# Performance work log

Hardware: AMD Instinct MI355X
Metric: run time of the kernel (lower is better)

Reference implementation:

```python
import jax, jax.numpy as jnp
import numpy as np

N_NODES = 100000
IN_DIM = 128
OUT_DIM = 128


def setup_inputs() -> dict:
    key = jax.random.key(0)
    ks = jax.random.split(key, 10)
    # entry counts must be multiples of the edge arity (shape)
    e1, e2, e3 = 300000, 600000, 600000  # arities 1, 2, 3 -> 300k/300k/200k hyperedges
    return {
        "x": jax.random.normal(ks[0], (N_NODES, IN_DIM), dtype=jnp.float32),
        "edge_idx_r1": jax.random.randint(ks[1], (2, e1), 0, N_NODES, dtype=jnp.int32),
        "edge_idx_r2": jax.random.randint(ks[2], (2, e2), 0, N_NODES, dtype=jnp.int32),
        "edge_idx_r3": jax.random.randint(ks[3], (2, e3), 0, N_NODES, dtype=jnp.int32),
        "A_r1": jax.random.normal(ks[4], (IN_DIM * 1, OUT_DIM), dtype=jnp.float32) * np.sqrt(2.0 / (IN_DIM * 1 + OUT_DIM)),
        "A_r2": jax.random.normal(ks[5], (IN_DIM * 2, OUT_DIM), dtype=jnp.float32) * np.sqrt(2.0 / (IN_DIM * 2 + OUT_DIM)),
        "A_r3": jax.random.normal(ks[6], (IN_DIM * 3, OUT_DIM), dtype=jnp.float32) * np.sqrt(2.0 / (IN_DIM * 3 + OUT_DIM)),
        "C_w": jax.random.normal(ks[7], (OUT_DIM, IN_DIM), dtype=jnp.float32) * (1.0 / np.sqrt(IN_DIM)),
        "C_b": jax.random.normal(ks[8], (OUT_DIM,), dtype=jnp.float32) * 0.01,
    }


def _edge_type_messages(x, edge_idx, A, arity, n_nodes):
    # edge_idx: [2, groups*arity]; row0 = src node ids, row1 reshaped -> dest = col 0
    dest = edge_idx[1].reshape(-1, arity)[:, 0]              # [groups]
    src = x[edge_idx[0]].reshape(-1, x.shape[1] * arity)     # [groups, in_dim*arity]
    msg = src @ A                                            # [groups, out_dim]
    # degree normalization within this edge type (== 1/counts from torch.unique)
    counts = jnp.zeros((n_nodes,), dtype=msg.dtype).at[dest].add(1.0)
    msg = msg * (1.0 / counts[dest])[:, None]
    return dest, msg


def reference(x, edge_idx_r1, edge_idx_r2, edge_idx_r3, A_r1, A_r2, A_r3, C_w, C_b):
    n = x.shape[0]
    agg = jnp.zeros((n, C_w.shape[0]), dtype=x.dtype)
    for ei, A, arity in ((edge_idx_r1, A_r1, 1), (edge_idx_r2, A_r2, 2), (edge_idx_r3, A_r3, 3)):
        dest, msg = _edge_type_messages(x, ei, A, arity, n)
        agg = agg.at[dest].add(msg)
    return x @ C_w.T + C_b + agg
```

## Files before the change

kernel.cpp:

```cpp
#include <hip/hip_runtime.h>

#define N_NODES 100000
#define DIM 128

typedef __attribute__((ext_vector_type(8))) short bf16x8;
typedef __attribute__((ext_vector_type(4))) float f32x4;
typedef __attribute__((ext_vector_type(8))) unsigned short ushort8;

__device__ __forceinline__ unsigned short f2bf(float f) {
    union { float f; unsigned u; } v; v.f = f;
    unsigned u = v.u + 0x7FFFu + ((v.u >> 16) & 1u);
    return (unsigned short)(u >> 16);
}
__device__ __forceinline__ float bl(unsigned u) { return __uint_as_float(u << 16); }
__device__ __forceinline__ float bh(unsigned u) { return __uint_as_float(u & 0xFFFF0000u); }

__device__ __forceinline__ void gload_lds16(const void* g, void* l) {
    __builtin_amdgcn_global_load_lds((const __attribute__((address_space(1))) void*)g,
                                     (__attribute__((address_space(3))) void*)l, 16, 0, 0);
}

__device__ __forceinline__ void acc2(float4& a, uint2 v) {
    a.x += bl(v.x); a.y += bh(v.x); a.z += bl(v.y); a.w += bh(v.y);
}
__device__ __forceinline__ void red4(float4& a) {
    a.x += __shfl_xor(a.x, 32); a.y += __shfl_xor(a.y, 32);
    a.z += __shfl_xor(a.z, 32); a.w += __shfl_xor(a.w, 32);
}
__device__ __forceinline__ uint2 pack4(float4 a) {
    uint2 r;
    r.x = (unsigned)f2bf(a.x) | ((unsigned)f2bf(a.y) << 16);
    r.y = (unsigned)f2bf(a.z) | ((unsigned)f2bf(a.w) << 16);
    return r;
}

__global__ void cvt_count_kernel(const float* __restrict__ x, unsigned short* __restrict__ xb,
                                 int n8, const int* __restrict__ e1d,
                                 const int* __restrict__ e2d, const int* __restrict__ e3d,
                                 int ng1, int ng12, int ngall, int* __restrict__ counts) {
    int i = blockIdx.x * 256 + threadIdx.x;
    if (i < n8) {
        const float4* p = reinterpret_cast<const float4*>(x) + (size_t)i * 2;
        float4 a = p[0], b = p[1];
        ushort8 o;
        o[0] = f2bf(a.x); o[1] = f2bf(a.y); o[2] = f2bf(a.z); o[3] = f2bf(a.w);
        o[4] = f2bf(b.x); o[5] = f2bf(b.y); o[6] = f2bf(b.z); o[7] = f2bf(b.w);
        *reinterpret_cast<ushort8*>(xb + (size_t)i * 8) = o;
    }
    if (i < ng1) atomicAdd(&counts[e1d[i]], 1);
    else if (i < ng12) atomicAdd(&counts[N_NODES + e2d[(size_t)(i - ng1) * 2]], 1);
    else if (i < ngall) atomicAdd(&counts[2 * N_NODES + e3d[(size_t)(i - ng12) * 3]], 1);
}

__global__ void cvt_B_all(const float* __restrict__ A1, const float* __restrict__ A2,
                          const float* __restrict__ A3, const float* __restrict__ Cw,
                          unsigned short* __restrict__ bts) {
    int kg = blockIdx.x;
    int c = threadIdx.x;
    float v;
    int slice, kp;
    if (kg < 128)      { slice = 0; kp = kg; v = A1[(size_t)kg * 128 + c]; }
    else if (kg < 384) { int k = kg - 128; slice = 1 + (k >> 7); kp = k & 127; v = A2[(size_t)k * 128 + c]; }
    else if (kg < 768) { int k = kg - 384; slice = 3 + (k >> 7); kp = k & 127; v = A3[(size_t)k * 128 + c]; }
    else               { int k = kg - 768; slice = 6; kp = k; v = Cw[(size_t)c * 128 + k]; }
    bts[(size_t)slice * 16384 + c * 128 + kp] = f2bf(v);
}

__global__ __launch_bounds__(256) void scan_p1(const int* __restrict__ counts,
                                               int* __restrict__ partials) {
    __shared__ int red[256];
    int type = blockIdx.y, blk = blockIdx.x, tid = threadIdx.x;
    int base = blk * 4096 + tid * 16;
    int s = 0;
#pragma unroll
    for (int j = 0; j < 16; ++j) {
        int i = base + j;
        s += (i < N_NODES) ? counts[(size_t)type * N_NODES + i] : 0;
    }
    red[tid] = s;
    __syncthreads();
    for (int off = 128; off > 0; off >>= 1) {
        if (tid < off) red[tid] += red[tid + off];
        __syncthreads();
    }
    if (tid == 0) partials[type * 32 + blk] = red[0];
}

__global__ __launch_bounds__(256) void scan_p3(const int* __restrict__ counts,
                                               const int* __restrict__ partials,
                                               int* __restrict__ cursor) {
    __shared__ int tsum[256];
    __shared__ int baseoff;
    int type = blockIdx.y, blk = blockIdx.x, tid = threadIdx.x;
    if (tid == 0) {
        int r = 0;
        for (int b = 0; b < blk; ++b) r += partials[type * 32 + b];
        baseoff = r;
    }
    int base = blk * 4096 + tid * 16;
    int v[16];
    int s = 0;
#pragma unroll
    for (int j = 0; j < 16; ++j) {
        int i = base + j;
        v[j] = (i < N_NODES) ? counts[(size_t)type * N_NODES + i] : 0;
        s += v[j];
    }
    tsum[tid] = s;
    __syncthreads();
    for (int off = 1; off < 256; off <<= 1) {
        int t2 = (tid >= off) ? tsum[tid - off] : 0;
        __syncthreads();
        tsum[tid] += t2;
        __syncthreads();
    }
    int run = tsum[tid] - s + baseoff;
#pragma unroll
    for (int j = 0; j < 16; ++j) {
        int i = base + j;
        if (i < N_NODES) cursor[(size_t)type * N_NODES + i] = run;
        run += v[j];
    }
}

__global__ void scatter_all_kernel(const int* __restrict__ e1, const int* __restrict__ e2,
                                   const int* __restrict__ e3, int ne1, int ne2, int ne3,
                                   int ng1, int ng12, int ngall, int* __restrict__ cursor,
                                   int* __restrict__ s1, int2* __restrict__ s2,
                                   int4* __restrict__ s3) {
    int g = blockIdx.x * 256 + threadIdx.x;
    if (g < ng1) {
        int d = e1[ne1 + g];
        s1[atomicAdd(&cursor[d], 1)] = e1[g];
    } else if (g < ng12) {
        int k = g - ng1;
        int d = e2[ne2 + 2 * (size_t)k];
        int2 v; v.x = e2[2 * (size_t)k]; v.y = e2[2 * (size_t)k + 1];
        s2[atomicAdd(&cursor[N_NODES + d], 1)] = v;
    } else if (g < ngall) {
        int k = g - ng12;
        int d = e3[ne3 + 3 * (size_t)k];
        int4 v; v.x = e3[3 * (size_t)k]; v.y = e3[3 * (size_t)k + 1];
        v.z = e3[3 * (size_t)k + 2]; v.w = 0;
        s3[atomicAdd(&cursor[2 * N_NODES + d], 1)] = v;
    }
}

__global__ __launch_bounds__(256) void aggregate_x_kernel(
    const unsigned short* __restrict__ xb,
    const int* __restrict__ s1, const int2* __restrict__ s2, const int4* __restrict__ s3,
    const int* __restrict__ counts, const int* __restrict__ ends,
    unsigned short* __restrict__ gbf)
{
    int d = blockIdx.x * 4 + (threadIdx.x >> 6);
    if (d >= N_NODES) return;
    const int l = threadIdx.x & 63, hw = l >> 5, sl = l & 31;
    float4 a0 = {0,0,0,0}, a1 = {0,0,0,0}, a2 = {0,0,0,0};
    float4 a3 = {0,0,0,0}, a4 = {0,0,0,0}, a5 = {0,0,0,0};

    int c1 = counts[d], c2 = counts[N_NODES + d], c3 = counts[2 * N_NODES + d];
    int e1e = ends[d], e2e = ends[N_NODES + d], e3e = ends[2 * N_NODES + d];

    if (c1) {
        for (int i = e1e - c1 + hw; i < e1e; i += 2) {
            uint2 v = *reinterpret_cast<const uint2*>(xb + (size_t)s1[i] * 128 + sl * 4);
            acc2(a0, v);
        }
        float inv = 1.f / (float)c1;
        a0.x *= inv; a0.y *= inv; a0.z *= inv; a0.w *= inv;
    }
    if (c2) {
        for (int i = e2e - c2 + hw; i < e2e; i += 2) {
            int2 p = s2[i];
            uint2 va = *reinterpret_cast<const uint2*>(xb + (size_t)p.x * 128 + sl * 4);
            uint2 vb = *reinterpret_cast<const uint2*>(xb + (size_t)p.y * 128 + sl * 4);
            acc2(a1, va); acc2(a2, vb);
        }
        float inv = 1.f / (float)c2;
        a1.x *= inv; a1.y *= inv; a1.z *= inv; a1.w *= inv;
        a2.x *= inv; a2.y *= inv; a2.z *= inv; a2.w *= inv;
    }
    if (c3) {
        for (int i = e3e - c3 + hw; i < e3e; i += 2) {
            int4 p = s3[i];
            uint2 va = *reinterpret_cast<const uint2*>(xb + (size_t)p.x * 128 + sl * 4);
            uint2 vb = *reinterpret_cast<const uint2*>(xb + (size_t)p.y * 128 + sl * 4);
            uint2 vc = *reinterpret_cast<const uint2*>(xb + (size_t)p.z * 128 + sl * 4);
            acc2(a3, va); acc2(a4, vb); acc2(a5, vc);
        }
        float inv = 1.f / (float)c3;
        a3.x *= inv; a3.y *= inv; a3.z *= inv; a3.w *= inv;
        a4.x *= inv; a4.y *= inv; a4.z *= inv; a4.w *= inv;
        a5.x *= inv; a5.y *= inv; a5.z *= inv; a5.w *= inv;
    }
    red4(a0); red4(a1); red4(a2); red4(a3); red4(a4); red4(a5);
    if (hw == 0) {
        *reinterpret_cast<uint2*>(gbf + ((size_t)0 * N_NODES + d) * 128 + sl * 4) = pack4(a0);
        *reinterpret_cast<uint2*>(gbf + ((size_t)1 * N_NODES + d) * 128 + sl * 4) = pack4(a1);
        *reinterpret_cast<uint2*>(gbf + ((size_t)2 * N_NODES + d) * 128 + sl * 4) = pack4(a2);
        *reinterpret_cast<uint2*>(gbf + ((size_t)3 * N_NODES + d) * 128 + sl * 4) = pack4(a3);
        *reinterpret_cast<uint2*>(gbf + ((size_t)4 * N_NODES + d) * 128 + sl * 4) = pack4(a4);
        *reinterpret_cast<uint2*>(gbf + ((size_t)5 * N_NODES + d) * 128 + sl * 4) = pack4(a5);
    }
}

__global__ __launch_bounds__(256, 2) void gemm_out_kernel(
    const unsigned short* __restrict__ xb, const unsigned short* __restrict__ gbf,
    const unsigned short* __restrict__ bts, const float* __restrict__ Cb,
    float* __restrict__ out, int nnodes)
{
    __shared__ __align__(16) char smem[65536];

    const int tid = threadIdx.x;
    const int w = tid >> 6, l = tid & 63;
    const int g0 = blockIdx.x * 128;
    const int lrow = l & 15, lk = l >> 4;
    const int wr = (w & 1) * 64, wc = (w >> 1) * 64;

    const int q = (((l & 7) ^ (l >> 3)) << 4);
    const int inner = q & 63;
    const int rpq = ((l >> 3) << 1) + (q >> 6);

    int aoff[4];
#pragma unroll
    for (int mi = 0; mi < 4; ++mi) {
        int r = wr + mi * 16 + lrow;
        int P = r >> 1;
        aoff[mi] = P * 128 + ((((r & 1) << 6) | (lk << 4)) ^ ((P & 7) << 4));
    }

    f32x4 acc[4][4];
#pragma unroll
    for (int mi = 0; mi < 4; ++mi)
#pragma unroll
        for (int ni = 0; ni < 4; ++ni) acc[mi][ni] = (f32x4){0.f, 0.f, 0.f, 0.f};

    auto STAGE = [&](int c, int buf) {
#pragma unroll
        for (int i = 0; i < 2; ++i) {
            int u = w * 2 + i;
            int r = u * 16 + rpq;
            int row = (g0 + r < nnodes) ? g0 + r : 0;
            const char* src = (c < 6)
                ? (const char*)gbf + ((size_t)c * N_NODES + row) * 256
                : (const char*)xb + (size_t)row * 256;
#pragma unroll
            for (int t2 = 0; t2 < 4; ++t2)
                gload_lds16(src + t2 * 64 + inner, smem + buf * 32768 + t2 * 8192 + u * 1024);
        }
    };

    STAGE(0, 0);
    asm volatile("s_waitcnt vmcnt(0)" ::: "memory");
    __builtin_amdgcn_s_barrier();
    asm volatile("" ::: "memory");

    for (int c = 0; c < 7; ++c) {
        if (c + 1 < 7) STAGE(c + 1, (c + 1) & 1);
        const int bb = (c & 1) * 32768;
#pragma unroll
        for (int ks = 0; ks < 4; ++ks) {
            bf16x8 af[4], bg[4];
#pragma unroll
            for (int mi = 0; mi < 4; ++mi)
                af[mi] = *reinterpret_cast<const bf16x8*>(smem + bb + ks * 8192 + aoff[mi]);
#pragma unroll
            for (int ni = 0; ni < 4; ++ni)
                bg[ni] = *reinterpret_cast<const bf16x8*>(
                    bts + (size_t)c * 16384 + (wc + ni * 16 + lrow) * 128 + ks * 32 + lk * 8);
            __builtin_amdgcn_s_setprio(1);
#pragma unroll
            for (int mi = 0; mi < 4; ++mi)
#pragma unroll
                for (int ni = 0; ni < 4; ++ni)
                    acc[mi][ni] = __builtin_amdgcn_mfma_f32_16x16x32_bf16(
                        af[mi], bg[ni], acc[mi][ni], 0, 0, 0);
            __builtin_amdgcn_s_setprio(0);
        }
        asm volatile("s_waitcnt vmcnt(0)" ::: "memory");
        __builtin_amdgcn_s_barrier();
        asm volatile("" ::: "memory");
    }

    float bv[4];
#pragma unroll
    for (int ni = 0; ni < 4; ++ni) bv[ni] = Cb[wc + ni * 16 + lrow];
#pragma unroll
    for (int mi = 0; mi < 4; ++mi)
#pragma unroll
        for (int reg = 0; reg < 4; ++reg) {
            int g = g0 + wr + mi * 16 + lk * 4 + reg;
            if (g < nnodes) {
#pragma unroll
                for (int ni = 0; ni < 4; ++ni)
                    out[(size_t)g * DIM + wc + ni * 16 + lrow] = acc[mi][ni][reg] + bv[ni];
            }
        }
}

extern "C" void kernel_launch(void* const* d_in, const int* in_sizes, int n_in,
                              void* d_out, int out_size, void* d_ws, size_t ws_size,
                              hipStream_t stream) {
    const float* x  = (const float*)d_in[0];
    const int*   e1 = (const int*)d_in[1];
    const int*   e2 = (const int*)d_in[2];
    const int*   e3 = (const int*)d_in[3];
    const float* A1 = (const float*)d_in[4];
    const float* A2 = (const float*)d_in[5];
    const float* A3 = (const float*)d_in[6];
    const float* Cw = (const float*)d_in[7];
    const float* Cb = (const float*)d_in[8];
    float* out = (float*)d_out;

    const int ne1 = in_sizes[1] / 2, ne2 = in_sizes[2] / 2, ne3 = in_sizes[3] / 2;
    const int ng1 = ne1, ng2 = ne2 / 2, ng3 = ne3 / 3;
    const int N = N_NODES;

    int*  counts  = (int*)d_ws;
    int*  cursor  = counts + 3 * N;
    int4* s3      = (int4*)(cursor + 3 * N);
    int2* s2      = (int2*)(s3 + ng3);
    int*  s1      = (int*)(s2 + ng2);
    int*  partials = s1 + ng1;
    unsigned short* bts = (unsigned short*)(partials + 128);
    unsigned short* xb  = bts + 7 * 16384;
    unsigned short* gbf = xb + (size_t)N * 128;

    const int ngall = ng1 + ng2 + ng3;
    const int n8 = N * DIM / 8;

    hipMemsetAsync(counts, 0, (size_t)3 * N * sizeof(int), stream);
    cvt_count_kernel<<<(n8 + 255) / 256, 256, 0, stream>>>(
        x, xb, n8, e1 + ne1, e2 + ne2, e3 + ne3, ng1, ng1 + ng2, ngall, counts);
    cvt_B_all<<<896, 128, 0, stream>>>(A1, A2, A3, Cw, bts);
    scan_p1<<<dim3(25, 3), 256, 0, stream>>>(counts, partials);
    scan_p3<<<dim3(25, 3), 256, 0, stream>>>(counts, partials, cursor);
    scatter_all_kernel<<<(ngall + 255) / 256, 256, 0, stream>>>(
        e1, e2, e3, ne1, ne2, ne3, ng1, ng1 + ng2, ngall, cursor, s1, s2, s3);
    aggregate_x_kernel<<<(N + 3) / 4, 256, 0, stream>>>(
        xb, s1, s2, s3, counts, cursor, gbf);
    gemm_out_kernel<<<(N + 127) / 128, 256, 0, stream>>>(xb, gbf, bts, Cb, out, N);
}
```

Baseline: 263.7 us.

## Fuse per-node gather aggregation into the output GEMM kernel via LDS staging

Replaces the separate aggregation kernel, which wrote six bf16 aggregated feature planes to global memory, and the GEMM that re-read them. Now each 128-node GEMM block gathers its own neighbor features (8 lanes per node, 16-byte loads, half the columns per pass), writes them as bf16 into swizzled LDS and immediately runs MFMAs against the matching weight slice. This removes the intermediate global write and read of roughly 150 MB. The cost is lower gather parallelism, since there are only about 782 blocks, each doing serialized per-node loops with barriers between phases, plus no overlap between gather and MFMA within a block.

Measured after the change: 337.3 us. 27.9% more time.

```diff
diff --git a/kernel.cpp b/kernel.cpp
--- a/kernel.cpp
+++ b/kernel.cpp
@@ -20,18 +20,18 @@
                                      (__attribute__((address_space(3))) void*)l, 16, 0, 0);
 }
 
-__device__ __forceinline__ void acc2(float4& a, uint2 v) {
+__device__ __forceinline__ void accum8(float4& a, float4& b, uint4 v) {
     a.x += bl(v.x); a.y += bh(v.x); a.z += bl(v.y); a.w += bh(v.y);
-}
-__device__ __forceinline__ void red4(float4& a) {
-    a.x += __shfl_xor(a.x, 32); a.y += __shfl_xor(a.y, 32);
-    a.z += __shfl_xor(a.z, 32); a.w += __shfl_xor(a.w, 32);
-}
-__device__ __forceinline__ uint2 pack4(float4 a) {
-    uint2 r;
-    r.x = (unsigned)f2bf(a.x) | ((unsigned)f2bf(a.y) << 16);
-    r.y = (unsigned)f2bf(a.z) | ((unsigned)f2bf(a.w) << 16);
-    return r;
+    b.x += bl(v.z); b.y += bh(v.z); b.z += bl(v.w); b.w += bh(v.w);
+}
+
+__device__ __forceinline__ void packwrite(void* dst, float4 a, float4 b, float inv) {
+    union { bf16x8 v; unsigned short u[8]; } r;
+    r.u[0] = f2bf(a.x * inv); r.u[1] = f2bf(a.y * inv);
+    r.u[2] = f2bf(a.z * inv); r.u[3] = f2bf(a.w * inv);
+    r.u[4] = f2bf(b.x * inv); r.u[5] = f2bf(b.y * inv);
+    r.u[6] = f2bf(b.z * inv); r.u[7] = f2bf(b.w * inv);
+    *reinterpret_cast<bf16x8*>(dst) = r.v;
 }
 
 __global__ void cvt_count_kernel(const float* __restrict__ x, unsigned short* __restrict__ xb,
@@ -146,76 +146,34 @@
     }
 }
 
-__global__ __launch_bounds__(256) void aggregate_x_kernel(
+__global__ __launch_bounds__(256, 3) void fused_agg_gemm_kernel(
     const unsigned short* __restrict__ xb,
     const int* __restrict__ s1, const int2* __restrict__ s2, const int4* __restrict__ s3,
     const int* __restrict__ counts, const int* __restrict__ ends,
-    unsigned short* __restrict__ gbf)
-{
-    int d = blockIdx.x * 4 + (threadIdx.x >> 6);
-    if (d >= N_NODES) return;
-    const int l = threadIdx.x & 63, hw = l >> 5, sl = l & 31;
-    float4 a0 = {0,0,0,0}, a1 = {0,0,0,0}, a2 = {0,0,0,0};
-    float4 a3 = {0,0,0,0}, a4 = {0,0,0,0}, a5 = {0,0,0,0};
-
-    int c1 = counts[d], c2 = counts[N_NODES + d], c3 = counts[2 * N_NODES + d];
-    int e1e = ends[d], e2e = ends[N_NODES + d], e3e = ends[2 * N_NODES + d];
-
-    if (c1) {
-        for (int i = e1e - c1 + hw; i < e1e; i += 2) {
-            uint2 v = *reinterpret_cast<const uint2*>(xb + (size_t)s1[i] * 128 + sl * 4);
-            acc2(a0, v);
-        }
-        float inv = 1.f / (float)c1;
-        a0.x *= inv; a0.y *= inv; a0.z *= inv; a0.w *= inv;
-    }
-    if (c2) {
-        for (int i = e2e - c2 + hw; i < e2e; i += 2) {
-            int2 p = s2[i];
-            uint2 va = *reinterpret_cast<const uint2*>(xb + (size_t)p.x * 128 + sl * 4);
-            uint2 vb = *reinterpret_cast<const uint2*>(xb + (size_t)p.y * 128 + sl * 4);
-            acc2(a1, va); acc2(a2, vb);
-        }
-        float inv = 1.f / (float)c2;
-        a1.x *= inv; a1.y *= inv; a1.z *= inv; a1.w *= inv;
-        a2.x *= inv; a2.y *= inv; a2.z *= inv; a2.w *= inv;
-    }
-    if (c3) {
-        for (int i = e3e - c3 + hw; i < e3e; i += 2) {
-            int4 p = s3[i];
-            uint2 va = *reinterpret_cast<const uint2*>(xb + (size_t)p.x * 128 + sl * 4);
-            uint2 vb = *reinterpret_cast<const uint2*>(xb + (size_t)p.y * 128 + sl * 4);
-            uint2 vc = *reinterpret_cast<const uint2*>(xb + (size_t)p.z * 128 + sl * 4);
-            acc2(a3, va); acc2(a4, vb); acc2(a5, vc);
-        }
-        float inv = 1.f / (float)c3;
-        a3.x *= inv; a3.y *= inv; a3.z *= inv; a3.w *= inv;
-        a4.x *= inv; a4.y *= inv; a4.z *= inv; a4.w *= inv;
-        a5.x *= inv; a5.y *= inv; a5.z *= inv; a5.w *= inv;
-    }
-    red4(a0); red4(a1); red4(a2); red4(a3); red4(a4); red4(a5);
-    if (hw == 0) {
-        *reinterpret_cast<uint2*>(gbf + ((size_t)0 * N_NODES + d) * 128 + sl * 4) = pack4(a0);
-        *reinterpret_cast<uint2*>(gbf + ((size_t)1 * N_NODES + d) * 128 + sl * 4) = pack4(a1);
-        *reinterpret_cast<uint2*>(gbf + ((size_t)2 * N_NODES + d) * 128 + sl * 4) = pack4(a2);
-        *reinterpret_cast<uint2*>(gbf + ((size_t)3 * N_NODES + d) * 128 + sl * 4) = pack4(a3);
-        *reinterpret_cast<uint2*>(gbf + ((size_t)4 * N_NODES + d) * 128 + sl * 4) = pack4(a4);
-        *reinterpret_cast<uint2*>(gbf + ((size_t)5 * N_NODES + d) * 128 + sl * 4) = pack4(a5);
-    }
-}
-
-__global__ __launch_bounds__(256, 2) void gemm_out_kernel(
-    const unsigned short* __restrict__ xb, const unsigned short* __restrict__ gbf,
     const unsigned short* __restrict__ bts, const float* __restrict__ Cb,
     float* __restrict__ out, int nnodes)
 {
-    __shared__ __align__(16) char smem[65536];
+    constexpr int CEOFF = 49152;
+    __shared__ __align__(16) char smem[49152 + 3072];
+    int* cntb = (int*)(smem + CEOFF);
+    int* endb = cntb + 384;
 
     const int tid = threadIdx.x;
     const int w = tid >> 6, l = tid & 63;
     const int g0 = blockIdx.x * 128;
     const int lrow = l & 15, lk = l >> 4;
     const int wr = (w & 1) * 64, wc = (w >> 1) * 64;
+    const int dg = l >> 3, ck = l & 7;
+
+    if (tid < 128) {
+        int d = g0 + tid;
+        bool ok = d < nnodes;
+#pragma unroll
+        for (int t = 0; t < 3; ++t) {
+            cntb[t * 128 + tid] = ok ? counts[(size_t)t * N_NODES + d] : 0;
+            endb[t * 128 + tid] = ok ? ends[(size_t)t * N_NODES + d] : 0;
+        }
+    }
 
     const int q = (((l & 7) ^ (l >> 3)) << 4);
     const int inner = q & 63;
@@ -235,39 +193,111 @@
 #pragma unroll
         for (int ni = 0; ni < 4; ++ni) acc[mi][ni] = (f32x4){0.f, 0.f, 0.f, 0.f};
 
-    auto STAGE = [&](int c, int buf) {
+    __syncthreads();
+
+    const char* xbB = (const char*)xb;
+
+#pragma unroll
+    for (int t = 0; t < 3; ++t) {
+#pragma unroll
+        for (int p = 0; p < 2; ++p) {
+            for (int sweep = 0; sweep < 4; ++sweep) {
+                const int dl = sweep * 32 + w * 8 + dg;
+                const int cnt = cntb[t * 128 + dl];
+                const int end = endb[t * 128 + dl];
+                const float inv = cnt ? 1.f / (float)cnt : 0.f;
+                const size_t coff = (size_t)p * 128 + ck * 16;
+                float4 a0 = {0,0,0,0}, a1 = {0,0,0,0};
+                float4 b0 = {0,0,0,0}, b1 = {0,0,0,0};
+                float4 c0 = {0,0,0,0}, c1 = {0,0,0,0};
+                if (t == 0) {
+                    for (int i = end - cnt; i < end; ++i) {
+                        uint4 v = *reinterpret_cast<const uint4*>(xbB + (size_t)s1[i] * 256 + coff);
+                        accum8(a0, a1, v);
+                    }
+                } else if (t == 1) {
+                    for (int i = end - cnt; i < end; ++i) {
+                        int2 pr = s2[i];
+                        uint4 va = *reinterpret_cast<const uint4*>(xbB + (size_t)pr.x * 256 + coff);
+                        uint4 vb = *reinterpret_cast<const uint4*>(xbB + (size_t)pr.y * 256 + coff);
+                        accum8(a0, a1, va);
+                        accum8(b0, b1, vb);
+                    }
+                } else {
+                    for (int i = end - cnt; i < end; ++i) {
+                        int4 pr = s3[i];
+                        uint4 va = *reinterpret_cast<const uint4*>(xbB + (size_t)pr.x * 256 + coff);
+                        uint4 vb = *reinterpret_cast<const uint4*>(xbB + (size_t)pr.y * 256 + coff);
+                        uint4 vc = *reinterpret_cast<const uint4*>(xbB + (size_t)pr.z * 256 + coff);
+                        accum8(a0, a1, va);
+                        accum8(b0, b1, vb);
+                        accum8(c0, c1, vc);
+                    }
+                }
+                const int P2 = dl >> 1;
+                const int base = (ck >> 2) * 8192 + P2 * 128 +
+                                 ((((dl & 1) << 6) | ((ck & 3) << 4)) ^ ((P2 & 7) << 4));
+                packwrite(smem + base, a0, a1, inv);
+                if (t >= 1) packwrite(smem + 16384 + base, b0, b1, inv);
+                if (t == 2) packwrite(smem + 32768 + base, c0, c1, inv);
+            }
+            __syncthreads();
+            const int sbase = (t == 0) ? 0 : (t == 1 ? 1 : 3);
+#pragma unroll
+            for (int qi = 0; qi < 3; ++qi) {
+                if (qi <= t) {
+                    const int sg = sbase + qi;
+#pragma unroll
+                    for (int ks = 0; ks < 2; ++ks) {
+                        bf16x8 af[4], bg[4];
+#pragma unroll
+                        for (int mi = 0; mi < 4; ++mi)
+                            af[mi] = *reinterpret_cast<const bf16x8*>(
+                                smem + qi * 16384 + ks * 8192 + aoff[mi]);
+#pragma unroll
+                        for (int ni = 0; ni < 4; ++ni)
+                            bg[ni] = *reinterpret_cast<const bf16x8*>(
+                                bts + (size_t)sg * 16384 + (wc + ni * 16 + lrow) * 128 +
+                                (p * 2 + ks) * 32 + lk * 8);
+                        __builtin_amdgcn_s_setprio(1);
+#pragma unroll
+                        for (int mi = 0; mi < 4; ++mi)
+#pragma unroll
+                            for (int ni = 0; ni < 4; ++ni)
+                                acc[mi][ni] = __builtin_amdgcn_mfma_f32_16x16x32_bf16(
+                                    af[mi], bg[ni], acc[mi][ni], 0, 0, 0);
+                        __builtin_amdgcn_s_setprio(0);
+                    }
+                }
+            }
+            __syncthreads();
+        }
+    }
+
+    {
 #pragma unroll
         for (int i = 0; i < 2; ++i) {
             int u = w * 2 + i;
             int r = u * 16 + rpq;
             int row = (g0 + r < nnodes) ? g0 + r : 0;
-            const char* src = (c < 6)
-                ? (const char*)gbf + ((size_t)c * N_NODES + row) * 256
-                : (const char*)xb + (size_t)row * 256;
+            const char* src = xbB + (size_t)row * 256;
 #pragma unroll
             for (int t2 = 0; t2 < 4; ++t2)
-                gload_lds16(src + t2 * 64 + inner, smem + buf * 32768 + t2 * 8192 + u * 1024);
-        }
-    };
-
-    STAGE(0, 0);
-    asm volatile("s_waitcnt vmcnt(0)" ::: "memory");
-    __builtin_amdgcn_s_barrier();
-    asm volatile("" ::: "memory");
-
-    for (int c = 0; c < 7; ++c) {
-        if (c + 1 < 7) STAGE(c + 1, (c + 1) & 1);
-        const int bb = (c & 1) * 32768;
+                gload_lds16(src + t2 * 64 + inner, smem + t2 * 8192 + u * 1024);
+        }
+        asm volatile("s_waitcnt vmcnt(0)" ::: "memory");
+        __builtin_amdgcn_s_barrier();
+        asm volatile("" ::: "memory");
 #pragma unroll
         for (int ks = 0; ks < 4; ++ks) {
             bf16x8 af[4], bg[4];
 #pragma unroll
             for (int mi = 0; mi < 4; ++mi)
-                af[mi] = *reinterpret_cast<const bf16x8*>(smem + bb + ks * 8192 + aoff[mi]);
+                af[mi] = *reinterpret_cast<const bf16x8*>(smem + ks * 8192 + aoff[mi]);
 #pragma unroll
             for (int ni = 0; ni < 4; ++ni)
                 bg[ni] = *reinterpret_cast<const bf16x8*>(
-                    bts + (size_t)c * 16384 + (wc + ni * 16 + lrow) * 128 + ks * 32 + lk * 8);
+                    bts + (size_t)6 * 16384 + (wc + ni * 16 + lrow) * 128 + ks * 32 + lk * 8);
             __builtin_amdgcn_s_setprio(1);
 #pragma unroll
             for (int mi = 0; mi < 4; ++mi)
@@ -277,9 +307,6 @@
                         af[mi], bg[ni], acc[mi][ni], 0, 0, 0);
             __builtin_amdgcn_s_setprio(0);
         }
-        asm volatile("s_waitcnt vmcnt(0)" ::: "memory");
-        __builtin_amdgcn_s_barrier();
-        asm volatile("" ::: "memory");
     }
 
     float bv[4];
@@ -324,7 +351,6 @@
     int*  partials = s1 + ng1;
     unsigned short* bts = (unsigned short*)(partials + 128);
     unsigned short* xb  = bts + 7 * 16384;
-    unsigned short* gbf = xb + (size_t)N * 128;
 
     const int ngall = ng1 + ng2 + ng3;
     const int n8 = N * DIM / 8;
@@ -337,7 +363,6 @@
     scan_p3<<<dim3(25, 3), 256, 0, stream>>>(counts, partials, cursor);
     scatter_all_kernel<<<(ngall + 255) / 256, 256, 0, stream>>>(
         e1, e2, e3, ne1, ne2, ne3, ng1, ng1 + ng2, ngall, cursor, s1, s2, s3);
-    aggregate_x_kernel<<<(N + 3) / 4, 256, 0, stream>>>(
-        xb, s1, s2, s3, counts, cursor, gbf);
-    gemm_out_kernel<<<(N + 127) / 128, 256, 0, stream>>>(xb, gbf, bts, Cb, out, N);
-}
+    fused_agg_gemm_kernel<<<(N + 127) / 128, 256, 0, stream>>>(
+        xb, s1, s2, s3, counts, cursor, bts, Cb, out, N);
+}
```
